# Performance work log

Hardware: AMD Instinct MI355X
Metric: run time of the kernel (lower is better)

The kernel has to match this reference:

```python
import jax, jax.numpy as jnp
import numpy as np

B, S, D, H = 4, 2048, 512, 8
DK = D // H


def setup_inputs() -> dict:
    key = jax.random.key(0)
    ks = jax.random.split(key, 12)
    s = 0.02
    return {
        "q": jax.random.normal(ks[0], (B, S, D), jnp.float32),
        "k": jax.random.normal(ks[1], (B, S, D), jnp.float32),
        "v": jax.random.normal(ks[2], (B, S, D), jnp.float32),
        "mask": jax.random.randint(ks[3], (B, 1, S, S), 0, 2, jnp.int32),
        "Wq": jax.random.normal(ks[4], (D, D), jnp.float32) * s,
        "bq": jnp.zeros((D,), jnp.float32),
        "Wk": jax.random.normal(ks[5], (D, D), jnp.float32) * s,
        "bk": jnp.zeros((D,), jnp.float32),
        "Wv": jax.random.normal(ks[6], (D, D), jnp.float32) * s,
        "bv": jnp.zeros((D,), jnp.float32),
        "Wo": jax.random.normal(ks[7], (D, D), jnp.float32) * s,
        "bo": jnp.zeros((D,), jnp.float32),
    }


def reference(q, k, v, mask, Wq, bq, Wk, bk, Wv, bv, Wo, bo):
    # Linear projections (torch Linear: x @ W.T + b)
    qh = (q @ Wq.T + bq).reshape(B, S, H, DK).transpose(0, 2, 1, 3)  # [B,H,S,dk]
    kh = (k @ Wk.T + bk).reshape(B, S, H, DK).transpose(0, 2, 1, 3)
    vh = (v @ Wv.T + bv).reshape(B, S, H, DK).transpose(0, 2, 1, 3)
    # FAITHFUL quirk: original divides by q.shape[1] AFTER transpose == num_heads
    scores = jnp.einsum("bhqd,bhkd->bhqk", qh, kh) / H  # [B,H,S,S]
    scores = jnp.where(mask == 0, jnp.float32(-1e9), scores)
    attn = jax.nn.softmax(scores, axis=-1)
    ctx = jnp.einsum("bhqk,bhkd->bhqd", attn, vh)  # [B,H,S,dk]
    x = ctx.transpose(0, 2, 1, 3).reshape(B, S, D)
    return x @ Wo.T + bo  # dropout is identity in eval mode
```

## Files before the change

kernel.cpp:

```cpp
#include <hip/hip_runtime.h>
#include <math.h>

constexpr int Bc  = 4;
constexpr int Sc  = 2048;
constexpr int Dc  = 512;
constexpr int Hc  = 8;
constexpr int DKc = 64;
constexpr int Mc  = Bc * Sc;

constexpr float SCALE_Q = 0.180336880111120426f;

typedef __attribute__((ext_vector_type(8)))  short s16x8;
typedef __attribute__((ext_vector_type(4)))  float f32x4;
typedef __attribute__((ext_vector_type(16))) float f32x16;

__device__ __forceinline__ unsigned short f2bf(float f) {
    __bf16 h = (__bf16)f;
    return __builtin_bit_cast(unsigned short, h);
}

__device__ __forceinline__ float fexp2(float x) {
#if __has_builtin(__builtin_amdgcn_exp2f)
    return __builtin_amdgcn_exp2f(x);
#else
    return __expf(x * 0.6931471805599453f);
#endif
}

__global__ __launch_bounds__(256)
void pack_mask(const int* __restrict__ mask, unsigned long long* __restrict__ out,
               int nwords)
{
    int gw   = (blockIdx.x * blockDim.x + threadIdx.x) >> 6;
    int lane = threadIdx.x & 63;
    int nw   = (gridDim.x * blockDim.x) >> 6;
    for (int w0 = gw * 4; w0 < nwords; w0 += nw * 4) {
        int vals[4];
#pragma unroll
        for (int c = 0; c < 4; ++c)
            vals[c] = mask[(size_t)(w0 + c) * 64 + lane];
#pragma unroll
        for (int c = 0; c < 4; ++c) {
            unsigned long long bits = __ballot(vals[c] != 0);
            if (lane == 0) out[w0 + c] = bits;
        }
    }
}

__global__ __launch_bounds__(256)
void cvt4(const float* __restrict__ i0, const float* __restrict__ i1,
          const float* __restrict__ i2, const float* __restrict__ i3,
          unsigned short* __restrict__ o0, unsigned short* __restrict__ o1,
          unsigned short* __restrict__ o2, unsigned short* __restrict__ o3,
          int n4)
{
    const float* in; unsigned short* out;
    switch (blockIdx.y) {
        case 0: in = i0; out = o0; break;
        case 1: in = i1; out = o1; break;
        case 2: in = i2; out = o2; break;
        default: in = i3; out = o3; break;
    }
    int i = blockIdx.x * 256 + threadIdx.x;
    if (i < n4) {
        float4 v = ((const float4*)in)[i];
        ushort4 r;
        r.x = f2bf(v.x); r.y = f2bf(v.y); r.z = f2bf(v.z); r.w = f2bf(v.w);
        ((ushort4*)out)[i] = r;
    }
}

__global__ __launch_bounds__(256, 3)
void gemm128(const unsigned short* __restrict__ x0, const unsigned short* __restrict__ x1,
             const unsigned short* __restrict__ x2,
             const unsigned short* __restrict__ w0, const unsigned short* __restrict__ w1,
             const unsigned short* __restrict__ w2,
             const float* __restrict__ b0, const float* __restrict__ b1,
             const float* __restrict__ b2,
             void* __restrict__ o0v, void* __restrict__ o1v, void* __restrict__ o2v,
             float s0, float s1, float s2, int m0, int m1, int m2)
{
    const unsigned short* X; const unsigned short* W; const float* bias; void* outv;
    float scale; int mode;
    switch (blockIdx.z) {
        case 0:  X = x0; W = w0; bias = b0; outv = o0v; scale = s0; mode = m0; break;
        case 1:  X = x1; W = w1; bias = b1; outv = o1v; scale = s1; mode = m1; break;
        default: X = x2; W = w2; bias = b2; outv = o2v; scale = s2; mode = m2; break;
    }

    __shared__ unsigned short Xs[2][128 * 64];
    __shared__ unsigned short Ws[2][64 * 64];

    const int tid = threadIdx.x;
    const int w = tid >> 6, lane = tid & 63, ln = lane & 15, qd = lane >> 4;
    const int wm = (w >> 1) * 64, wn = (w & 1) * 32;
    const int row0 = blockIdx.x * 128, col0 = blockIdx.y * 64;

    f32x4 acc[4][2];
#pragma unroll
    for (int mt = 0; mt < 4; ++mt)
#pragma unroll
        for (int nt = 0; nt < 2; ++nt) acc[mt][nt] = f32x4{0.f, 0.f, 0.f, 0.f};

    auto stage = [&](int buf, int k0) {
#pragma unroll
        for (int c = 0; c < 4; ++c) {
            const int s = c * 256 + w * 64 + lane;
            const int r = s >> 3, cc = (s & 7) ^ (r & 7);
            const unsigned short* gs = X + (size_t)(row0 + r) * 512 + k0 + cc * 8;
            __builtin_amdgcn_global_load_lds(
                (const __attribute__((address_space(1))) unsigned int*)gs,
                (__attribute__((address_space(3))) unsigned int*)
                    ((char*)&Xs[buf][0] + (c * 256 + w * 64) * 16),
                16, 0, 0);
        }
#pragma unroll
        for (int c = 0; c < 2; ++c) {
            const int s = c * 256 + w * 64 + lane;
            const int r = s >> 3, cc = (s & 7) ^ (r & 7);
            const unsigned short* gs = W + (size_t)(col0 + r) * 512 + k0 + cc * 8;
            __builtin_amdgcn_global_load_lds(
                (const __attribute__((address_space(1))) unsigned int*)gs,
                (__attribute__((address_space(3))) unsigned int*)
                    ((char*)&Ws[buf][0] + (c * 256 + w * 64) * 16),
                16, 0, 0);
        }
    };

    stage(0, 0);
    for (int k0 = 0; k0 < 512; k0 += 64) {
        const int buf = (k0 >> 6) & 1;
        __syncthreads();
        if (k0 + 64 < 512) stage(buf ^ 1, k0 + 64);
#pragma unroll
        for (int kc = 0; kc < 2; ++kc) {
            s16x8 af[4], bfr[2];
#pragma unroll
            for (int mt = 0; mt < 4; ++mt) {
                int r = wm + mt * 16 + ln;
                af[mt] = *(const s16x8*)&Xs[buf][r * 64 + (((kc * 4 + qd) ^ (ln & 7)) * 8)];
            }
#pragma unroll
            for (int nt = 0; nt < 2; ++nt) {
                int r = wn + nt * 16 + ln;
                bfr[nt] = *(const s16x8*)&Ws[buf][r * 64 + (((kc * 4 + qd) ^ (ln & 7)) * 8)];
            }
#pragma unroll
            for (int mt = 0; mt < 4; ++mt)
#pragma unroll
                for (int nt = 0; nt < 2; ++nt)
                    acc[mt][nt] = __builtin_amdgcn_mfma_f32_16x16x32_bf16(
                        af[mt], bfr[nt], acc[mt][nt], 0, 0, 0);
        }
    }

#pragma unroll
    for (int nt = 0; nt < 2; ++nt) {
        const int n = col0 + wn + nt * 16 + ln;
        const float bz = bias[n];
#pragma unroll
        for (int mt = 0; mt < 4; ++mt) {
            const int mbase = row0 + wm + mt * 16 + qd * 4;
            if (mode == 0) {
                float* o = (float*)outv;
#pragma unroll
                for (int r = 0; r < 4; ++r)
                    o[(size_t)(mbase + r) * 512 + n] = acc[mt][nt][r] + bz;
            } else if (mode == 1) {
                unsigned short* o = (unsigned short*)outv;
                const int h = n >> 6, dk = n & 63;
#pragma unroll
                for (int r = 0; r < 4; ++r) {
                    int m = mbase + r, b = m >> 11, s = m & 2047;
                    o[((size_t)(b * Hc + h) * Sc + s) * 64 + dk] =
                        f2bf((acc[mt][nt][r] + bz) * scale);
                }
            } else {
                unsigned short* o = (unsigned short*)outv;
                const int h = n >> 6, dk = n & 63;
                const int b = mbase >> 11, sb = mbase & 2047;
                const int ss = (sb & ~12) | ((sb & 4) << 1) | ((sb & 8) >> 1);
                ushort4 pk;
                pk.x = f2bf((acc[mt][nt][0] + bz) * scale);
                pk.y = f2bf((acc[mt][nt][1] + bz) * scale);
                pk.z = f2bf((acc[mt][nt][2] + bz) * scale);
                pk.w = f2bf((acc[mt][nt][3] + bz) * scale);
                *(ushort4*)(o + ((size_t)(b * Hc + h) * 64 + dk) * Sc + ss) = pk;
            }
        }
    }
}

__global__ __launch_bounds__(256, 4)
void attn_mfma(const unsigned short* __restrict__ qh, const unsigned short* __restrict__ kh,
               const unsigned short* __restrict__ vt, const unsigned* __restrict__ mbits,
               unsigned short* __restrict__ ctx)
{
    __shared__ uint4 smem4[2][1024];

    const int bh = blockIdx.y, b = bh >> 3, h = bh & 7;
    const int q0 = blockIdx.x * 64;
    const int tid = threadIdx.x;
    const int w = tid >> 6;
    const int g = w >> 1;
    const int kh_ = w & 1;
    const int lane = tid & 63, ln = lane & 31, hf = lane >> 5;
    const int wv = tid >> 7;
    const int qr = q0 + g * 32 + ln;

    s16x8 qf[4];
    {
        const unsigned short* qp = qh + ((size_t)bh * Sc + qr) * 64 + hf * 8;
#pragma unroll
        for (int kc = 0; kc < 4; ++kc)
            qf[kc] = *(const s16x8*)(qp + kc * 16);
    }

    f32x16 o0, o1;
#pragma unroll
    for (int r = 0; r < 16; ++r) { o0[r] = 0.f; o1[r] = 0.f; }
    float lr = 0.f;

    const unsigned* mr = mbits + ((size_t)b * Sc + qr) * (Sc / 32);
    const unsigned short* kbase = kh + (size_t)bh * Sc * 64;
    const unsigned short* vbase = vt + (size_t)bh * 64 * Sc;

    const int kt0 = kh_ * 1024;

    auto stage_tile = [&](int buf, int kt) {
        char* gb = (char*)smem4[buf] + kh_ * 8192;
#pragma unroll
        for (int c = 0; c < 2; ++c) {
            const int seg = wv * 2 + c;
            const int s   = seg * 64 + lane;
            const int r   = s >> 3, cc = (s & 7) ^ (r & 7);
            const unsigned short* gs = kbase + (size_t)(kt + r) * 64 + cc * 8;
            __builtin_amdgcn_global_load_lds(
                (const __attribute__((address_space(1))) unsigned int*)gs,
                (__attribute__((address_space(3))) unsigned int*)(gb + seg * 1024),
                16, 0, 0);
        }
        char* vb = gb + 4096;
#pragma unroll
        for (int c = 0; c < 2; ++c) {
            const int seg = wv * 2 + c;
            const int dv  = lane ^ (seg << 1);
            const unsigned short* gs = vbase + (size_t)dv * Sc + kt + seg * 8;
            __builtin_amdgcn_global_load_lds(
                (const __attribute__((address_space(1))) unsigned int*)gs,
                (__attribute__((address_space(3))) unsigned int*)(vb + seg * 1024),
                16, 0, 0);
        }
    };

    stage_tile(0, kt0);
    unsigned mwn = mr[kt0 >> 5];

    for (int i = 0; i < 32; ++i) {
        const int kt = kt0 + i * 32;
        const int buf = i & 1;
        __syncthreads();
        const unsigned mw = mwn;
        if (i < 31) {
            stage_tile(buf ^ 1, kt + 32);
            mwn = mr[(kt + 32) >> 5];
        }

        const unsigned short* Ks = (const unsigned short*)smem4[buf] + kh_ * 4096;
        const unsigned short* Vs = Ks + 2048;

        f32x16 sv;
#pragma unroll
        for (int r = 0; r < 16; ++r) sv[r] = 0.f;
        __builtin_amdgcn_s_setprio(1);
#pragma unroll
        for (int kc = 0; kc < 4; ++kc) {
            s16x8 kf = *(const s16x8*)&Ks[ln * 64 + ((((kc << 1) | hf) ^ (ln & 7)) * 8)];
            sv = __builtin_amdgcn_mfma_f32_32x32x16_bf16(kf, qf[kc], sv, 0, 0, 0);
        }
        __builtin_amdgcn_s_setprio(0);

        float ps = 0.f;
        unsigned pu[8];
#pragma unroll
        for (int r = 0; r < 16; r += 2) {
            int key0 = (r & 3) + 8 * (r >> 2) + 4 * hf;
            int key1 = ((r + 1) & 3) + 8 * ((r + 1) >> 2) + 4 * hf;
            float a0 = ((mw >> key0) & 1u) ? sv[r]     : -1e9f;
            float a1 = ((mw >> key1) & 1u) ? sv[r + 1] : -1e9f;
            float p0 = fexp2(a0), p1 = fexp2(a1);
            ps += p0 + p1;
            pu[r >> 1] = (unsigned)f2bf(p0) | ((unsigned)f2bf(p1) << 16);
        }
        lr += ps;

        __builtin_amdgcn_s_setprio(1);
#pragma unroll
        for (int kc = 0; kc < 2; ++kc) {
            uint4 ua; ua.x = pu[4*kc]; ua.y = pu[4*kc+1]; ua.z = pu[4*kc+2]; ua.w = pu[4*kc+3];
            s16x8 pf = __builtin_bit_cast(s16x8, ua);
            const int cc = (kc << 1) | hf;
            s16x8 v0  = *(const s16x8*)&Vs[(cc * 64 + (ln ^ (cc << 1))) * 8];
            s16x8 v1  = *(const s16x8*)&Vs[(cc * 64 + ((32 + ln) ^ (cc << 1))) * 8];
            o0 = __builtin_amdgcn_mfma_f32_32x32x16_bf16(v0, pf, o0, 0, 0, 0);
            o1 = __builtin_amdgcn_mfma_f32_32x32x16_bf16(v1, pf, o1, 0, 0, 0);
        }
        __builtin_amdgcn_s_setprio(0);
    }

    lr += __shfl_xor(lr, 32);

    __syncthreads();
    float* cs = (float*)smem4[0];
    const int row = g * 64 + lane;
    float* my = cs + (size_t)row * 48;
    const int sw = lane & 7;
    if (kh_ == 1) {
#pragma unroll
        for (int r = 0; r < 4; ++r) {
            *(float4*)(my + ((r ^ sw) * 4))       = make_float4(o0[4*r], o0[4*r+1], o0[4*r+2], o0[4*r+3]);
            *(float4*)(my + (((r + 4) ^ sw) * 4)) = make_float4(o1[4*r], o1[4*r+1], o1[4*r+2], o1[4*r+3]);
        }
        my[32] = lr;
    }
    __syncthreads();
    if (kh_ == 0) {
        lr += my[32];
        const float inv = 1.f / lr;
#pragma unroll
        for (int r = 0; r < 4; ++r) {
            float4 a0 = *(const float4*)(my + ((r ^ sw) * 4));
            float4 a1 = *(const float4*)(my + (((r + 4) ^ sw) * 4));
            o0[4*r]   = (o0[4*r]   + a0.x) * inv; o0[4*r+1] = (o0[4*r+1] + a0.y) * inv;
            o0[4*r+2] = (o0[4*r+2] + a0.z) * inv; o0[4*r+3] = (o0[4*r+3] + a0.w) * inv;
            o1[4*r]   = (o1[4*r]   + a1.x) * inv; o1[4*r+1] = (o1[4*r+1] + a1.y) * inv;
            o1[4*r+2] = (o1[4*r+2] + a1.z) * inv; o1[4*r+3] = (o1[4*r+3] + a1.w) * inv;
        }
        unsigned short* op = ctx + ((size_t)(b * Sc + qr)) * 512 + h * 64;
#pragma unroll
        for (int gg = 0; gg < 4; ++gg) {
            ushort4 a, c;
            a.x = f2bf(o0[gg*4+0]); a.y = f2bf(o0[gg*4+1]);
            a.z = f2bf(o0[gg*4+2]); a.w = f2bf(o0[gg*4+3]);
            c.x = f2bf(o1[gg*4+0]); c.y = f2bf(o1[gg*4+1]);
            c.z = f2bf(o1[gg*4+2]); c.w = f2bf(o1[gg*4+3]);
            *(ushort4*)(op + 8 * gg + 4 * hf)      = a;
            *(ushort4*)(op + 32 + 8 * gg + 4 * hf) = c;
        }
    }
}

extern "C" void kernel_launch(void* const* d_in, const int* in_sizes, int n_in,
                              void* d_out, int out_size, void* d_ws, size_t ws_size,
                              hipStream_t stream)
{
    (void)in_sizes; (void)n_in; (void)out_size; (void)ws_size;

    const float* q    = (const float*)d_in[0];
    const float* k    = (const float*)d_in[1];
    const float* v    = (const float*)d_in[2];
    const int*   mask = (const int*)  d_in[3];
    const float* Wq   = (const float*)d_in[4];
    const float* bq   = (const float*)d_in[5];
    const float* Wk   = (const float*)d_in[6];
    const float* bk   = (const float*)d_in[7];
    const float* Wv   = (const float*)d_in[8];
    const float* bv   = (const float*)d_in[9];
    const float* Wo   = (const float*)d_in[10];
    const float* bo   = (const float*)d_in[11];
    float* out = (float*)d_out;

    constexpr size_t TEN = (size_t)Bc * Hc * Sc * DKc;
    char* p = (char*)d_ws;
    unsigned short* wqb   = (unsigned short*)p;  p += (size_t)Dc * Dc * 2;
    unsigned short* wkb   = (unsigned short*)p;  p += (size_t)Dc * Dc * 2;
    unsigned short* wvb   = (unsigned short*)p;  p += (size_t)Dc * Dc * 2;
    unsigned short* wob   = (unsigned short*)p;  p += (size_t)Dc * Dc * 2;
    unsigned short* qh_bf = (unsigned short*)p;  p += TEN * 2;
    unsigned short* kh_bf = (unsigned short*)p;  p += TEN * 2;
    unsigned short* vt_bf = (unsigned short*)p;  p += TEN * 2;
    unsigned short* ctx   = (unsigned short*)p;  p += TEN * 2;
    unsigned long long* mb64 = (unsigned long long*)p;

    unsigned short* qb = (unsigned short*)d_out;
    unsigned short* kb = qb + TEN;
    unsigned short* vb = ctx;

    const int nwords = Bc * Sc * (Sc / 64);

    dim3 bb(256);

    pack_mask<<<dim3(16384), bb, 0, stream>>>(mask, mb64, nwords);
    cvt4<<<dim3(Dc * Dc / 4 / 256, 4), bb, 0, stream>>>(Wq, Wk, Wv, Wo, wqb, wkb, wvb, wob,
                                                        Dc * Dc / 4);
    cvt4<<<dim3((int)(TEN / 4 / 256), 3), bb, 0, stream>>>(q, k, v, v, qb, kb, vb, vb,
                                                           (int)(TEN / 4));
    gemm128<<<dim3(Mc / 128, Dc / 64, 3), bb, 0, stream>>>(
        qb, kb, vb, wqb, wkb, wvb, bq, bk, bv, qh_bf, kh_bf, vt_bf,
        SCALE_Q, 1.0f, 1.0f, 1, 1, 2);
    attn_mfma<<<dim3(Sc / 64, Bc * Hc), bb, 0, stream>>>(qh_bf, kh_bf, vt_bf,
                                                         (const unsigned*)mb64, ctx);
    gemm128<<<dim3(Mc / 128, Dc / 64, 1), bb, 0, stream>>>(
        ctx, ctx, ctx, wob, wob, wob, bo, bo, bo, out, out, out,
        1.0f, 1.0f, 1.0f, 0, 0, 0);
}
```

Baseline: 269.4 us.

## Stage projection epilogue through LDS for coalesced stores and remap attention blocks

The projection GEMM epilogue for the bf16 head-major Q/K and transposed V outputs now writes results into shared memory first. Each thread then issues wide 16-byte global stores of contiguous rows, replacing scattered 2-byte and 8-byte writes. The attention kernel also remaps its block index so consecutive workgroups land on different XCDs while each XCD handles contiguous query tiles of the same head, aiming for better L2 reuse of K/V. The cost is two extra barriers and LDS traffic in the epilogue, and the code assumes the block tile fits the padded LDS layout.

```diff
diff --git a/kernel.cpp b/kernel.cpp
--- a/kernel.cpp
+++ b/kernel.cpp
@@ -154,40 +154,81 @@
         }
     }
 
-#pragma unroll
-    for (int nt = 0; nt < 2; ++nt) {
-        const int n = col0 + wn + nt * 16 + ln;
-        const float bz = bias[n];
-#pragma unroll
-        for (int mt = 0; mt < 4; ++mt) {
-            const int mbase = row0 + wm + mt * 16 + qd * 4;
-            if (mode == 0) {
+    if (mode == 0) {
+#pragma unroll
+        for (int nt = 0; nt < 2; ++nt) {
+            const int n = col0 + wn + nt * 16 + ln;
+            const float bz = bias[n];
+#pragma unroll
+            for (int mt = 0; mt < 4; ++mt) {
+                const int mbase = row0 + wm + mt * 16 + qd * 4;
                 float* o = (float*)outv;
 #pragma unroll
                 for (int r = 0; r < 4; ++r)
                     o[(size_t)(mbase + r) * 512 + n] = acc[mt][nt][r] + bz;
-            } else if (mode == 1) {
-                unsigned short* o = (unsigned short*)outv;
-                const int h = n >> 6, dk = n & 63;
-#pragma unroll
-                for (int r = 0; r < 4; ++r) {
-                    int m = mbase + r, b = m >> 11, s = m & 2047;
-                    o[((size_t)(b * Hc + h) * Sc + s) * 64 + dk] =
-                        f2bf((acc[mt][nt][r] + bz) * scale);
-                }
-            } else {
-                unsigned short* o = (unsigned short*)outv;
-                const int h = n >> 6, dk = n & 63;
-                const int b = mbase >> 11, sb = mbase & 2047;
-                const int ss = (sb & ~12) | ((sb & 4) << 1) | ((sb & 8) >> 1);
-                ushort4 pk;
-                pk.x = f2bf((acc[mt][nt][0] + bz) * scale);
-                pk.y = f2bf((acc[mt][nt][1] + bz) * scale);
-                pk.z = f2bf((acc[mt][nt][2] + bz) * scale);
-                pk.w = f2bf((acc[mt][nt][3] + bz) * scale);
-                *(ushort4*)(o + ((size_t)(b * Hc + h) * 64 + dk) * Sc + ss) = pk;
             }
         }
+    } else if (mode == 1) {
+        __syncthreads();
+        unsigned short* T = &Xs[0][0];
+#pragma unroll
+        for (int nt = 0; nt < 2; ++nt) {
+            const int n = col0 + wn + nt * 16 + ln;
+            const float bz = bias[n];
+            const int dk = n & 63;
+#pragma unroll
+            for (int mt = 0; mt < 4; ++mt) {
+                const int ml = wm + mt * 16 + qd * 4;
+#pragma unroll
+                for (int r = 0; r < 4; ++r)
+                    T[(ml + r) * 72 + dk] = f2bf((acc[mt][nt][r] + bz) * scale);
+            }
+        }
+        __syncthreads();
+        const int sl = tid >> 1, halfo = (tid & 1) * 32;
+        const int h = col0 >> 6, bb = row0 >> 11, sm = row0 & 2047;
+        const unsigned short* Tr = &T[sl * 72 + halfo];
+        uint4 d0 = *(const uint4*)(Tr);
+        uint4 d1 = *(const uint4*)(Tr + 8);
+        uint4 d2 = *(const uint4*)(Tr + 16);
+        uint4 d3 = *(const uint4*)(Tr + 24);
+        unsigned short* o = (unsigned short*)outv +
+                            ((size_t)(bb * Hc + h) * Sc + sm + sl) * 64 + halfo;
+        *(uint4*)(o)      = d0;
+        *(uint4*)(o + 8)  = d1;
+        *(uint4*)(o + 16) = d2;
+        *(uint4*)(o + 24) = d3;
+    } else {
+        __syncthreads();
+        unsigned short* T2 = &Xs[0][0];
+#pragma unroll
+        for (int nt = 0; nt < 2; ++nt) {
+            const int n = col0 + wn + nt * 16 + ln;
+            const float bz = bias[n];
+            const int dk = n & 63;
+#pragma unroll
+            for (int mt = 0; mt < 4; ++mt) {
+                const int ml = wm + mt * 16 + qd * 4;
+                const int sw = (ml & ~12) | ((ml & 4) << 1) | ((ml & 8) >> 1);
+#pragma unroll
+                for (int r = 0; r < 4; ++r)
+                    T2[dk * 136 + sw + r] = f2bf((acc[mt][nt][r] + bz) * scale);
+            }
+        }
+        __syncthreads();
+        const int dv = tid >> 2, qo = (tid & 3) * 32;
+        const int h = col0 >> 6, bb = row0 >> 11, sm = row0 & 2047;
+        const unsigned short* Tr = &T2[dv * 136 + qo];
+        uint4 d0 = *(const uint4*)(Tr);
+        uint4 d1 = *(const uint4*)(Tr + 8);
+        uint4 d2 = *(const uint4*)(Tr + 16);
+        uint4 d3 = *(const uint4*)(Tr + 24);
+        unsigned short* o = (unsigned short*)outv +
+                            ((size_t)(bb * Hc + h) * 64 + dv) * Sc + sm + qo;
+        *(uint4*)(o)      = d0;
+        *(uint4*)(o + 8)  = d1;
+        *(uint4*)(o + 16) = d2;
+        *(uint4*)(o + 24) = d3;
     }
 }
 
@@ -198,8 +239,11 @@
 {
     __shared__ uint4 smem4[2][1024];
 
-    const int bh = blockIdx.y, b = bh >> 3, h = bh & 7;
-    const int q0 = blockIdx.x * 64;
+    const int pwg = blockIdx.y * gridDim.x + blockIdx.x;
+    const int lg  = (pwg & 7) * 128 + (pwg >> 3);
+    const int bh = lg >> 5, b = bh >> 3, h = bh & 7;
+    const int q0 = (lg & 31) * 64;
+
     const int tid = threadIdx.x;
     const int w = tid >> 6;
     const int g = w >> 1;
```

Result: no change. 265.7 us (-1.4%).
